# Kernel tuning notes

Measured on AMD Instinct MI355X. Metric: run time of the kernel, lower is better.

## Reference

```python
import jax, jax.numpy as jnp
import numpy as np

B, NPG, K, H = 64, 2048, 10, 64   # graphs, points-per-graph, kNN, hidden
N = B * NPG
EPS = 1e-5  # PairNorm eps


def _lin_init(key, fan_in, fan_out):
    kw, kb = jax.random.split(key)
    s = 1.0 / np.sqrt(fan_in)
    W = jax.random.uniform(kw, (fan_in, fan_out), jnp.float32, -s, s)
    b = jax.random.uniform(kb, (fan_out,), jnp.float32, -s, s)
    return W, b


def setup_inputs() -> dict:
    key = jax.random.key(0)
    ks = jax.random.split(key, 6)
    pos = jax.random.normal(ks[0], (N, 2), jnp.float32)
    batch = jnp.repeat(jnp.arange(B, dtype=jnp.int32), NPG)
    W1, b1 = _lin_init(ks[1], 2, H)
    W2, b2 = _lin_init(ks[2], H + 2, H)
    W3, b3 = _lin_init(ks[3], H + 2, H)
    Wl1, bl1 = _lin_init(ks[4], H, H)
    Wl2, bl2 = _lin_init(ks[5], H, 2)
    return dict(pos=pos, batch=batch, W1=W1, b1=b1, W2=W2, b2=b2,
                W3=W3, b3=b3, Wl1=Wl1, bl1=bl1, Wl2=Wl2, bl2=bl2)


def pair_norm(x):
    # PyG PairNorm, mode='PN', scale=1: center, then divide by rms of row norms
    xc = x - x.mean(axis=0, keepdims=True)
    return xc / jnp.sqrt(EPS + (xc ** 2).sum(axis=-1).mean())


def knn_edges(pos):
    # equal-sized graphs laid out contiguously -> batched pairwise distances
    p = pos.reshape(B, NPG, 2)
    d2 = ((p[:, :, None, :] - p[:, None, :, :]) ** 2).sum(-1)   # [B, n, n]
    d2 = jnp.where(jnp.eye(NPG, dtype=bool), jnp.inf, d2)       # loop=False
    _, idx = jax.lax.top_k(-d2, K)                              # [B, n, K]
    offs = (jnp.arange(NPG * B, step=NPG) if False else (jnp.arange(B) * NPG))[:, None, None]
    src = (idx + offs).reshape(-1)                              # neighbor j
    dst = jnp.broadcast_to(jnp.arange(N).reshape(B, NPG, 1), (B, NPG, K)).reshape(-1)
    # PointNetConv(add_self_loops=True): append self edges once, reuse in all convs
    sl = jnp.arange(N)
    return jnp.concatenate([src, sl]), jnp.concatenate([dst, sl])


def pointnet_conv(x, pos, src, dst, W, b):
    rel = pos[src] - pos[dst]                                    # [E, 2]
    msg = rel if x is None else jnp.concatenate([x[src], rel], axis=-1)
    msg = msg @ W + b                                            # local_nn
    return jax.ops.segment_max(msg, dst, num_segments=N)         # aggr='max'


def reference(pos, batch, W1, b1, W2, b2, W3, b3, Wl1, bl1, Wl2, bl2):
    src, dst = knn_edges(pos)
    h1 = pair_norm(jax.nn.relu(pointnet_conv(None, pos, src, dst, W1, b1)))
    h2 = pair_norm(jax.nn.relu(pointnet_conv(h1, pos, src, dst, W2, b2)))
    h3 = pair_norm(jax.nn.relu(pointnet_conv(h2, pos, src, dst, W3, b3)))
    g = h3.reshape(B, NPG, H).max(axis=1)                        # global_max_pool
    g = jax.nn.relu(g @ Wl1 + bl1)
    # dropout p=0.2 is identity in eval mode
    return g @ Wl2 + bl2                                         # [B, 2]
```

## Files before the change

### kernel.cpp

```cpp
#include <hip/hip_runtime.h>
#include <math.h>

#define NTOT   131072
#define NPG    2048
#define NB     64
#define KNNK   10
#define HID    64
#define EPSPN  1e-5f

__device__ inline float rdlane(float v, int l) {
    return __int_as_float(__builtin_amdgcn_readlane(__float_as_int(v), l));
}

__global__ __launch_bounds__(1024) void sort_kernel(const float2* __restrict__ pos,
        float2* __restrict__ spos, unsigned short* __restrict__ y2xg)
{
    __shared__ float2   sp[NPG];
    __shared__ unsigned sk[NPG];
    __shared__ unsigned sv[NPG];
    const int base = blockIdx.x * NPG;
    const int tid  = threadIdx.x;

    for (int t = tid; t < NPG; t += 1024) {
        unsigned u = __float_as_uint(pos[base + t].x);
        sk[t] = (u & 0x80000000u) ? ~u : (u | 0x80000000u);
        sv[t] = (unsigned)t;
    }
    __syncthreads();
    for (int k = 2; k <= NPG; k <<= 1) {
        for (int j = k >> 1; j > 0; j >>= 1) {
            int i = ((tid & ~(j - 1)) << 1) | (tid & (j - 1));
            int l = i + j;
            bool up = ((i & k) == 0);
            unsigned a = sk[i], b = sk[l];
            if ((a > b) == up) {
                sk[i] = b; sk[l] = a;
                unsigned t2 = sv[i]; sv[i] = sv[l]; sv[l] = t2;
            }
            __syncthreads();
        }
    }
    for (int t = tid; t < NPG; t += 1024) sp[t] = pos[base + sv[t]];
    __syncthreads();
    for (int t = tid; t < NPG; t += 1024) spos[base + t] = sp[t];

    for (int t = tid; t < NPG; t += 1024) {
        unsigned u = __float_as_uint(sp[t].y);
        sk[t] = (u & 0x80000000u) ? ~u : (u | 0x80000000u);
        sv[t] = (unsigned)t;
    }
    __syncthreads();
    for (int k = 2; k <= NPG; k <<= 1) {
        for (int j = k >> 1; j > 0; j >>= 1) {
            int i = ((tid & ~(j - 1)) << 1) | (tid & (j - 1));
            int l = i + j;
            bool up = ((i & k) == 0);
            unsigned a = sk[i], b = sk[l];
            if ((a > b) == up) {
                sk[i] = b; sk[l] = a;
                unsigned t2 = sv[i]; sv[i] = sv[l]; sv[l] = t2;
            }
            __syncthreads();
        }
    }
    for (int t = tid; t < NPG; t += 1024) y2xg[base + t] = (unsigned short)sv[t];
}

#define INSERT(INS, D2, JJ) do {                                              \
    const bool ins_ = (INS);                                                  \
    bd[9] = ins_ ? (D2) : bd[9];                                              \
    bi[9] = ins_ ? (JJ) : bi[9];                                              \
    _Pragma("unroll")                                                         \
    for (int kk = 0; kk < 9; ++kk) {                                          \
        bool sw_ = bd[kk] > bd[9];                                            \
        float tv_ = bd[kk]; int ti_ = bi[kk];                                 \
        bd[kk] = sw_ ? bd[9] : bd[kk]; bi[kk] = sw_ ? bi[9] : bi[kk];         \
        bd[9]  = sw_ ? tv_  : bd[9];   bi[9]  = sw_ ? ti_  : bi[9];           \
    }                                                                         \
} while (0)

#define CSWAP(A, B) do {                                                      \
    bool sw_ = bd[A] > bd[B];                                                 \
    float tf_ = bd[A]; int ti_ = bi[A];                                       \
    bd[A] = sw_ ? bd[B] : bd[A]; bi[A] = sw_ ? bi[B] : bi[A];                 \
    bd[B] = sw_ ? tf_  : bd[B]; bi[B] = sw_ ? ti_  : bi[B];                   \
} while (0)

__global__ __launch_bounds__(256) void knn_kernel(const float2* __restrict__ spos,
        const unsigned short* __restrict__ y2xg, unsigned short* __restrict__ knn)
{
    __shared__ float2 sarr[NPG];
    __shared__ unsigned short y2x[NPG];
    __shared__ unsigned short x2y[NPG];
    const int tid  = threadIdx.x;
    const int g    = blockIdx.x >> 4;
    const int base = g * NPG;

    for (int t = tid; t < NPG; t += 256) {
        sarr[t] = spos[base + t];
        y2x[t]  = y2xg[base + t];
    }
    __syncthreads();
    for (int t = tid; t < NPG; t += 256) {
        x2y[(int)y2x[t]] = (unsigned short)t;
    }
    __syncthreads();

    const int ql = ((blockIdx.x & 15) << 7) + (tid >> 1);
    const int d  = tid & 1;
    const float qx = sarr[ql].x, qy = sarr[ql].y;
    const int py = (int)x2y[ql];

    float span_x = sarr[min(ql + 8, NPG - 1)].x - sarr[max(ql - 8, 0)].x;
    float span_y = sarr[(int)y2x[min(py + 8, NPG - 1)]].y
                 - sarr[(int)y2x[max(py - 8, 0)]].y;
    const bool cy   = span_y > span_x;
    const int  r    = cy ? py : ql;
    const int  limit = d ? (NPG - 1 - r) : r;
    const int  sign  = d ? 1 : -1;

    float bd[KNNK];
    int   bi[KNNK];
#pragma unroll
    for (int k = 0; k < KNNK; ++k) { bd[k] = INFINITY; bi[k] = 0; }

    int s = 1;
    bool alive = (limit >= 1);
    while (__any(alive)) {
        int j0 = min(NPG - 1, max(0, r + sign * s));
        int j1 = min(NPG - 1, max(0, r + sign * (s + 1)));
        int j2 = min(NPG - 1, max(0, r + sign * (s + 2)));
        int j3 = min(NPG - 1, max(0, r + sign * (s + 3)));
        int x0 = cy ? (int)y2x[j0] : j0;
        int x1 = cy ? (int)y2x[j1] : j1;
        int x2 = cy ? (int)y2x[j2] : j2;
        int x3 = cy ? (int)y2x[j3] : j3;
        float2 p0 = sarr[x0];
        float2 p1 = sarr[x1];
        float2 p2 = sarr[x2];
        float2 p3 = sarr[x3];
        float dx0 = __fsub_rn(qx, p0.x), dy0 = __fsub_rn(qy, p0.y);
        float dx1 = __fsub_rn(qx, p1.x), dy1 = __fsub_rn(qy, p1.y);
        float dx2 = __fsub_rn(qx, p2.x), dy2 = __fsub_rn(qy, p2.y);
        float dx3 = __fsub_rn(qx, p3.x), dy3 = __fsub_rn(qy, p3.y);
        float xs0 = __fmul_rn(dx0, dx0), ys0 = __fmul_rn(dy0, dy0);
        float xs1 = __fmul_rn(dx1, dx1), ys1 = __fmul_rn(dy1, dy1);
        float xs2 = __fmul_rn(dx2, dx2), ys2 = __fmul_rn(dy2, dy2);
        float xs3 = __fmul_rn(dx3, dx3), ys3 = __fmul_rn(dy3, dy3);
        float d20 = __fadd_rn(xs0, ys0);
        float d21 = __fadd_rn(xs1, ys1);
        float d22 = __fadd_rn(xs2, ys2);
        float d23 = __fadd_rn(xs3, ys3);
        bool v0 = alive && (s     <= limit);
        bool v1 = alive && (s + 1 <= limit);
        bool v2 = alive && (s + 2 <= limit);
        bool v3 = alive && (s + 3 <= limit);
        bool pre = (v0 && d20 < bd[9]) || (v1 && d21 < bd[9]) ||
                   (v2 && d22 < bd[9]) || (v3 && d23 < bd[9]);
        if (__any(pre)) {
            INSERT(v0 && (d20 < bd[9]), d20, x0);
            INSERT(v1 && (d21 < bd[9]), d21, x1);
            INSERT(v2 && (d22 < bd[9]), d22, x2);
            INSERT(v3 && (d23 < bd[9]), d23, x3);
        }
        float thr = fminf(bd[9], __shfl_xor(bd[9], 1));
        float pr3 = cy ? ys3 : xs3;
        alive = alive && (s + 4 <= limit) && (pr3 < thr);
        s += 4;
    }

#pragma unroll
    for (int ph = 0; ph < 10; ++ph) {
        if ((ph & 1) == 0) { CSWAP(0,1); CSWAP(2,3); CSWAP(4,5); CSWAP(6,7); CSWAP(8,9); }
        else               { CSWAP(1,2); CSWAP(3,4); CSWAP(5,6); CSWAP(7,8); }
    }
    float obd[KNNK]; int obi[KNNK];
#pragma unroll
    for (int k = 0; k < KNNK; ++k) {
        obd[k] = __shfl_xor(bd[k], 1);
        obi[k] = __shfl_xor(bi[k], 1);
    }
    if (d == 0) {
        const int row = (base + ql) * KNNK;
#pragma unroll
        for (int k = 0; k < KNNK; ++k) {
            bool ta = bd[k] < obd[9 - k];
            int idx = ta ? bi[k] : obi[9 - k];
            knn[row + k] = (unsigned short)idx;
        }
    }
}

#define GEMM64(V, OUTEXPR) do {                                               \
    float a0 = 0.f, a1 = 0.f, a2 = 0.f, a3 = 0.f;                             \
    _Pragma("unroll")                                                         \
    for (int k = 0; k < 16; ++k) {                                            \
        a0 = fmaf(rdlane((V), k),      wcol[k],      a0);                     \
        a1 = fmaf(rdlane((V), k + 16), wcol[k + 16], a1);                     \
        a2 = fmaf(rdlane((V), k + 32), wcol[k + 32], a2);                     \
        a3 = fmaf(rdlane((V), k + 48), wcol[k + 48], a3);                     \
    }                                                                         \
    (OUTEXPR) = (a0 + a1) + (a2 + a3);                                        \
} while (0)

#define WSWZ() (((blockIdx.x & 7) << 7) | (blockIdx.x >> 3))

__global__ __launch_bounds__(256) void conv1_kernel(const float2* __restrict__ spos,
        const unsigned short* __restrict__ knn, const float* __restrict__ W1,
        const float* __restrict__ b1, const float* __restrict__ W2a,
        float* __restrict__ out, float* __restrict__ st)
{
    __shared__ float red[256];
    const int tid  = threadIdx.x;
    const int lane = tid & 63, w = tid >> 6;
    const int wg   = WSWZ();
    const int i0   = wg * 128 + w * 32;
    const int base = (wg >> 4) << 11;
    const float w0 = W1[lane], w1 = W1[HID + lane], bb = b1[lane];
    float wcol[HID];
#pragma unroll
    for (int k = 0; k < HID; ++k) wcol[k] = W2a[k * HID + lane];
    float cs = 0.f, ss = 0.f;
    for (int r = 0; r < 32; ++r) {
        const int i = i0 + r;
        float2 pi = spos[i];
        float acc = bb;
#pragma unroll
        for (int e = 0; e < KNNK; ++e) {
            int j = base + (int)knn[i * KNNK + e];
            float2 pj = spos[j];
            acc = fmaxf(acc, fmaf(pj.x - pi.x, w0, fmaf(pj.y - pi.y, w1, bb)));
        }
        float v = fmaxf(acc, 0.f);
        cs += v; ss = fmaf(v, v, ss);
        GEMM64(v, out[(size_t)i * HID + lane]);
    }
    red[tid] = cs; __syncthreads();
    if (tid < 64) atomicAdd(&st[tid], red[tid] + red[tid + 64] + red[tid + 128] + red[tid + 192]);
#pragma unroll
    for (int o = 32; o > 0; o >>= 1) ss += __shfl_xor(ss, o, 64);
    __syncthreads();
    if (lane == 0) red[w] = ss;
    __syncthreads();
    if (tid == 0) atomicAdd(&st[64], red[0] + red[1] + red[2] + red[3]);
}

__global__ __launch_bounds__(64) void stats_kernel(float* __restrict__ st,
        const float* __restrict__ Wn, const float* __restrict__ bn)
{
    const int c = threadIdx.x;
    float mean = st[c] * (1.0f / (float)NTOT);
    st[128 + c] = mean;
    float m2 = mean * mean;
#pragma unroll
    for (int o = 32; o > 0; o >>= 1) m2 += __shfl_xor(m2, o, 64);
    float s = (st[64] - (float)NTOT * m2) * (1.0f / (float)NTOT);
    s = fmaxf(s, 0.f);
    float inv = 1.0f / sqrtf(EPSPN + s);
    if (c == 0) st[66] = inv;
    if (Wn != nullptr) {
        float dot = 0.f;
#pragma unroll
        for (int k = 0; k < HID; ++k) dot = fmaf(rdlane(mean, k), Wn[k * HID + c], dot);
        st[192 + c] = bn[c] - inv * dot;
    }
}

__global__ __launch_bounds__(256, 2) void convG2_kernel(const float2* __restrict__ spos,
        const unsigned short* __restrict__ knn, const float* __restrict__ hw,
        const float* __restrict__ Wb, const float* __restrict__ Wna,
        const float* __restrict__ stin, float* __restrict__ out,
        float* __restrict__ stout)
{
    __shared__ float red[256];
    const int tid  = threadIdx.x;
    const int lane = tid & 63, w = tid >> 6;
    const int wg   = WSWZ();
    const int i0   = wg * 128 + w * 32;
    const int base = (wg >> 4) << 11;
    const float wb0 = Wb[lane], wb1 = Wb[HID + lane];
    const float inv = stin[66], offs = stin[192 + lane];
    float wcol[HID];
#pragma unroll
    for (int k = 0; k < HID; ++k) wcol[k] = Wna[k * HID + lane];

    const unsigned* kb = (const unsigned*)knn;
    unsigned idx0[5], idx1[5];
    float hwC[KNNK], hwN[KNNK];
#pragma unroll
    for (int e = 0; e < 5; ++e) idx0[e] = kb[(size_t)i0 * 5 + e];
#pragma unroll
    for (int e = 0; e < 5; ++e) idx1[e] = kb[(size_t)(i0 + 1) * 5 + e];
#pragma unroll
    for (int e = 0; e < 5; ++e) {
        int ja = base + (int)(idx0[e] & 0xFFFFu);
        int jb = base + (int)(idx0[e] >> 16);
        hwC[2 * e]     = hw[(size_t)ja * HID + lane];
        hwC[2 * e + 1] = hw[(size_t)jb * HID + lane];
    }

    float cs = 0.f, ss = 0.f;
    for (int r = 0; r < 32; ++r) {
        const int i = i0 + r;
        unsigned idx2[5];
        if (r + 2 < 32) {
#pragma unroll
            for (int e = 0; e < 5; ++e) idx2[e] = kb[(size_t)(i + 2) * 5 + e];
        }
        float2 pi = spos[i];
        float acc = fmaf(inv, hw[(size_t)i * HID + lane], offs);
#pragma unroll
        for (int e = 0; e < 5; ++e) {
            int ja = base + (int)(idx0[e] & 0xFFFFu);
            int jb = base + (int)(idx0[e] >> 16);
            float2 pa = spos[ja];
            float2 pb = spos[jb];
            float xwa = fmaf(inv, hwC[2 * e],     offs);
            float xwb = fmaf(inv, hwC[2 * e + 1], offs);
            acc = fmaxf(acc, fmaf(pa.x - pi.x, wb0, fmaf(pa.y - pi.y, wb1, xwa)));
            acc = fmaxf(acc, fmaf(pb.x - pi.x, wb0, fmaf(pb.y - pi.y, wb1, xwb)));
        }
        if (r + 1 < 32) {
#pragma unroll
            for (int e = 0; e < 5; ++e) {
                int ja = base + (int)(idx1[e] & 0xFFFFu);
                int jb = base + (int)(idx1[e] >> 16);
                hwN[2 * e]     = hw[(size_t)ja * HID + lane];
                hwN[2 * e + 1] = hw[(size_t)jb * HID + lane];
            }
        }
        float v = fmaxf(acc, 0.f);
        cs += v; ss = fmaf(v, v, ss);
        GEMM64(v, out[(size_t)i * HID + lane]);
#pragma unroll
        for (int e = 0; e < 5; ++e) idx0[e] = idx1[e];
        if (r + 2 < 32) {
#pragma unroll
            for (int e = 0; e < 5; ++e) idx1[e] = idx2[e];
        }
#pragma unroll
        for (int e = 0; e < KNNK; ++e) hwC[e] = hwN[e];
    }
    red[tid] = cs; __syncthreads();
    if (tid < 64) atomicAdd(&stout[tid], red[tid] + red[tid + 64] + red[tid + 128] + red[tid + 192]);
#pragma unroll
    for (int o = 32; o > 0; o >>= 1) ss += __shfl_xor(ss, o, 64);
    __syncthreads();
    if (lane == 0) red[w] = ss;
    __syncthreads();
    if (tid == 0) atomicAdd(&stout[64], red[0] + red[1] + red[2] + red[3]);
}

__global__ __launch_bounds__(256, 2) void convB3_kernel(const float2* __restrict__ spos,
        const unsigned short* __restrict__ knn, const float* __restrict__ hw,
        const float* __restrict__ Wb, const float* __restrict__ stin,
        float* __restrict__ stout, float* __restrict__ gmax)
{
    __shared__ float red[256];
    const int tid  = threadIdx.x;
    const int lane = tid & 63, w = tid >> 6;
    const int wg   = WSWZ();
    const int i0   = wg * 128 + w * 32;
    const int base = (wg >> 4) << 11;
    const float wb0 = Wb[lane], wb1 = Wb[HID + lane];
    const float inv = stin[66], offs = stin[192 + lane];

    const unsigned* kb = (const unsigned*)knn;
    unsigned idx0[5], idx1[5];
    float hwC[KNNK], hwN[KNNK];
#pragma unroll
    for (int e = 0; e < 5; ++e) idx0[e] = kb[(size_t)i0 * 5 + e];
#pragma unroll
    for (int e = 0; e < 5; ++e) idx1[e] = kb[(size_t)(i0 + 1) * 5 + e];
#pragma unroll
    for (int e = 0; e < 5; ++e) {
        int ja = base + (int)(idx0[e] & 0xFFFFu);
        int jb = base + (int)(idx0[e] >> 16);
        hwC[2 * e]     = hw[(size_t)ja * HID + lane];
        hwC[2 * e + 1] = hw[(size_t)jb * HID + lane];
    }

    float cs = 0.f, ss = 0.f, gm = 0.f;
    for (int r = 0; r < 32; ++r) {
        const int i = i0 + r;
        unsigned idx2[5];
        if (r + 2 < 32) {
#pragma unroll
            for (int e = 0; e < 5; ++e) idx2[e] = kb[(size_t)(i + 2) * 5 + e];
        }
        float2 pi = spos[i];
        float acc = fmaf(inv, hw[(size_t)i * HID + lane], offs);
#pragma unroll
        for (int e = 0; e < 5; ++e) {
            int ja = base + (int)(idx0[e] & 0xFFFFu);
            int jb = base + (int)(idx0[e] >> 16);
            float2 pa = spos[ja];
            float2 pb = spos[jb];
            float xwa = fmaf(inv, hwC[2 * e],     offs);
            float xwb = fmaf(inv, hwC[2 * e + 1], offs);
            acc = fmaxf(acc, fmaf(pa.x - pi.x, wb0, fmaf(pa.y - pi.y, wb1, xwa)));
            acc = fmaxf(acc, fmaf(pb.x - pi.x, wb0, fmaf(pb.y - pi.y, wb1, xwb)));
        }
        if (r + 1 < 32) {
#pragma unroll
            for (int e = 0; e < 5; ++e) {
                int ja = base + (int)(idx1[e] & 0xFFFFu);
                int jb = base + (int)(idx1[e] >> 16);
                hwN[2 * e]     = hw[(size_t)ja * HID + lane];
                hwN[2 * e + 1] = hw[(size_t)jb * HID + lane];
            }
        }
        float v = fmaxf(acc, 0.f);
        cs += v; ss = fmaf(v, v, ss);
        gm = fmaxf(gm, v);
#pragma unroll
        for (int e = 0; e < 5; ++e) idx0[e] = idx1[e];
        if (r + 2 < 32) {
#pragma unroll
            for (int e = 0; e < 5; ++e) idx1[e] = idx2[e];
        }
#pragma unroll
        for (int e = 0; e < KNNK; ++e) hwC[e] = hwN[e];
    }
    red[tid] = cs; __syncthreads();
    if (tid < 64) atomicAdd(&stout[tid], red[tid] + red[tid + 64] + red[tid + 128] + red[tid + 192]);
#pragma unroll
    for (int o = 32; o > 0; o >>= 1) ss += __shfl_xor(ss, o, 64);
    __syncthreads();
    if (lane == 0) red[w] = ss;
    __syncthreads();
    if (tid == 0) atomicAdd(&stout[64], red[0] + red[1] + red[2] + red[3]);
    const int g = (wg >> 4);
    atomicMax((int*)gmax + g * HID + lane, __float_as_int(gm));
}

__global__ __launch_bounds__(64) void head_kernel(const float* __restrict__ gmax,
        const float* __restrict__ st3, const float* __restrict__ Wl1,
        const float* __restrict__ bl1, const float* __restrict__ Wl2,
        const float* __restrict__ bl2, float* __restrict__ out)
{
    const int b = blockIdx.x, c = threadIdx.x;
    float gv = (gmax[b * HID + c] - st3[128 + c]) * st3[66];
    float a = bl1[c];
#pragma unroll
    for (int k = 0; k < HID; ++k) a = fmaf(rdlane(gv, k), Wl1[k * HID + c], a);
    float h1 = fmaxf(a, 0.f);
    float o = bl2[c & 1];
#pragma unroll
    for (int k = 0; k < HID; ++k) o = fmaf(rdlane(h1, k), Wl2[k * 2 + (c & 1)], o);
    if (c < 2) out[b * 2 + c] = o;
}

extern "C" void kernel_launch(void* const* d_in, const int* in_sizes, int n_in,
                              void* d_out, int out_size, void* d_ws, size_t ws_size,
                              hipStream_t stream)
{
    const float2* pos = (const float2*)d_in[0];
    const float* W1  = (const float*)d_in[2];
    const float* b1  = (const float*)d_in[3];
    const float* W2  = (const float*)d_in[4];
    const float* b2  = (const float*)d_in[5];
    const float* W3  = (const float*)d_in[6];
    const float* b3  = (const float*)d_in[7];
    const float* Wl1 = (const float*)d_in[8];
    const float* bl1 = (const float*)d_in[9];
    const float* Wl2 = (const float*)d_in[10];
    const float* bl2 = (const float*)d_in[11];
    float* out = (float*)d_out;

    char* p = (char*)d_ws;
    unsigned short* knn  = (unsigned short*)p;  p += (size_t)NTOT * KNNK * 2;
    float2* spos = (float2*)p;                  p += (size_t)NTOT * 8;
    unsigned short* y2xg = (unsigned short*)p;  p += (size_t)NTOT * 2;
    float* bufA  = (float*)p;                   p += (size_t)NTOT * HID * 4;
    float* bufB  = (float*)p;                   p += (size_t)NTOT * HID * 4;
    float* st    = (float*)p;
    float* gmax  = st + 768;

    hipMemsetAsync(st, 0, (768 + NB * HID) * sizeof(float), stream);

    sort_kernel<<<NB, 1024, 0, stream>>>(pos, spos, y2xg);
    knn_kernel <<<NTOT / 128, 256, 0, stream>>>(spos, y2xg, knn);

    conv1_kernel<<<NTOT / 128, 256, 0, stream>>>(spos, knn, W1, b1, W2, bufA, st);
    stats_kernel<<<1, 64, 0, stream>>>(st, W2, b2);

    convG2_kernel<<<NTOT / 128, 256, 0, stream>>>(spos, knn, bufA, W2 + 64 * HID,
                                                  W3, st, bufB, st + 256);
    stats_kernel<<<1, 64, 0, stream>>>(st + 256, W3, b3);

    convB3_kernel<<<NTOT / 128, 256, 0, stream>>>(spos, knn, bufB, W3 + 64 * HID,
                                                  st + 256, st + 512, gmax);
    stats_kernel<<<1, 64, 0, stream>>>(st + 512, nullptr, nullptr);

    head_kernel<<<NB, 64, 0, stream>>>(gmax, st + 512, Wl1, bl1, Wl2, bl2, out);
}
```

Baseline: 348.7 us.

## Split kNN sweep across four lanes per query with interleaved stride phases

Each query now uses four lanes instead of two: two directions times two interleaved phases, each phase stepping by eight along the sorted axis. The per-lane top-10 lists are combined with two sort-and-bitonic-min-merge rounds over xor-1 and xor-2 shuffles, and the grid doubles to 64 queries per block. The single batched insert check is also split into per-candidate wave-uniform insert guards. This shortens each lane's serial scan and adds parallelism, at the cost of restaging the whole graph's shared memory in twice as many blocks and doing an extra sort/merge.

```diff
diff --git a/kernel.cpp b/kernel.cpp
--- a/kernel.cpp
+++ b/kernel.cpp
@@ -86,6 +86,34 @@
     bd[B] = sw_ ? tf_  : bd[B]; bi[B] = sw_ ? ti_  : bi[B];                   \
 } while (0)
 
+#define SORT10() do {                                                         \
+    _Pragma("unroll")                                                         \
+    for (int ph_ = 0; ph_ < 10; ++ph_) {                                      \
+        if ((ph_ & 1) == 0) { CSWAP(0,1); CSWAP(2,3); CSWAP(4,5);             \
+                              CSWAP(6,7); CSWAP(8,9); }                       \
+        else                { CSWAP(1,2); CSWAP(3,4); CSWAP(5,6);             \
+                              CSWAP(7,8); }                                   \
+    }                                                                         \
+} while (0)
+
+#define MINMERGE(XORW) do {                                                   \
+    float obd[KNNK]; int obi[KNNK];                                           \
+    _Pragma("unroll")                                                         \
+    for (int k = 0; k < KNNK; ++k) {                                          \
+        obd[k] = __shfl_xor(bd[k], (XORW));                                   \
+        obi[k] = __shfl_xor(bi[k], (XORW));                                   \
+    }                                                                         \
+    float nbd[KNNK]; int nbi[KNNK];                                           \
+    _Pragma("unroll")                                                         \
+    for (int k = 0; k < KNNK; ++k) {                                          \
+        bool ta = bd[k] < obd[9 - k];                                         \
+        nbd[k] = ta ? bd[k] : obd[9 - k];                                     \
+        nbi[k] = ta ? bi[k] : obi[9 - k];                                     \
+    }                                                                         \
+    _Pragma("unroll")                                                         \
+    for (int k = 0; k < KNNK; ++k) { bd[k] = nbd[k]; bi[k] = nbi[k]; }        \
+} while (0)
+
 __global__ __launch_bounds__(256) void knn_kernel(const float2* __restrict__ spos,
         const unsigned short* __restrict__ y2xg, unsigned short* __restrict__ knn)
 {
@@ -93,7 +121,7 @@
     __shared__ unsigned short y2x[NPG];
     __shared__ unsigned short x2y[NPG];
     const int tid  = threadIdx.x;
-    const int g    = blockIdx.x >> 4;
+    const int g    = blockIdx.x >> 5;
     const int base = g * NPG;
 
     for (int t = tid; t < NPG; t += 256) {
@@ -106,8 +134,10 @@
     }
     __syncthreads();
 
-    const int ql = ((blockIdx.x & 15) << 7) + (tid >> 1);
-    const int d  = tid & 1;
+    const int ql = ((blockIdx.x & 31) << 6) + (tid >> 2);
+    const int d  = tid & 3;
+    const int dir = d & 1;
+    const int ph  = d >> 1;
     const float qx = sarr[ql].x, qy = sarr[ql].y;
     const int py = (int)x2y[ql];
 
@@ -116,8 +146,8 @@
                  - sarr[(int)y2x[max(py - 8, 0)]].y;
     const bool cy   = span_y > span_x;
     const int  r    = cy ? py : ql;
-    const int  limit = d ? (NPG - 1 - r) : r;
-    const int  sign  = d ? 1 : -1;
+    const int  limit = dir ? (NPG - 1 - r) : r;
+    const int  sign  = dir ? 1 : -1;
 
     float bd[KNNK];
     int   bi[KNNK];
@@ -125,12 +155,13 @@
     for (int k = 0; k < KNNK; ++k) { bd[k] = INFINITY; bi[k] = 0; }
 
     int s = 1;
-    bool alive = (limit >= 1);
+    bool alive = (4 * ph + 1 <= limit);
     while (__any(alive)) {
-        int j0 = min(NPG - 1, max(0, r + sign * s));
-        int j1 = min(NPG - 1, max(0, r + sign * (s + 1)));
-        int j2 = min(NPG - 1, max(0, r + sign * (s + 2)));
-        int j3 = min(NPG - 1, max(0, r + sign * (s + 3)));
+        const int o0 = s + 4 * ph;
+        int j0 = min(NPG - 1, max(0, r + sign * o0));
+        int j1 = min(NPG - 1, max(0, r + sign * (o0 + 1)));
+        int j2 = min(NPG - 1, max(0, r + sign * (o0 + 2)));
+        int j3 = min(NPG - 1, max(0, r + sign * (o0 + 3)));
         int x0 = cy ? (int)y2x[j0] : j0;
         int x1 = cy ? (int)y2x[j1] : j1;
         int x2 = cy ? (int)y2x[j2] : j2;
@@ -151,43 +182,36 @@
         float d21 = __fadd_rn(xs1, ys1);
         float d22 = __fadd_rn(xs2, ys2);
         float d23 = __fadd_rn(xs3, ys3);
-        bool v0 = alive && (s     <= limit);
-        bool v1 = alive && (s + 1 <= limit);
-        bool v2 = alive && (s + 2 <= limit);
-        bool v3 = alive && (s + 3 <= limit);
-        bool pre = (v0 && d20 < bd[9]) || (v1 && d21 < bd[9]) ||
-                   (v2 && d22 < bd[9]) || (v3 && d23 < bd[9]);
-        if (__any(pre)) {
-            INSERT(v0 && (d20 < bd[9]), d20, x0);
-            INSERT(v1 && (d21 < bd[9]), d21, x1);
-            INSERT(v2 && (d22 < bd[9]), d22, x2);
-            INSERT(v3 && (d23 < bd[9]), d23, x3);
-        }
+        bool v0 = alive && (o0     <= limit);
+        bool v1 = alive && (o0 + 1 <= limit);
+        bool v2 = alive && (o0 + 2 <= limit);
+        bool v3 = alive && (o0 + 3 <= limit);
+        bool c0 = v0 && (d20 < bd[9]);
+        if (__any(c0)) INSERT(c0, d20, x0);
+        bool c1 = v1 && (d21 < bd[9]);
+        if (__any(c1)) INSERT(c1, d21, x1);
+        bool c2 = v2 && (d22 < bd[9]);
+        if (__any(c2)) INSERT(c2, d22, x2);
+        bool c3 = v3 && (d23 < bd[9]);
+        if (__any(c3)) INSERT(c3, d23, x3);
+
         float thr = fminf(bd[9], __shfl_xor(bd[9], 1));
+        thr = fminf(thr, __shfl_xor(thr, 2));
         float pr3 = cy ? ys3 : xs3;
-        alive = alive && (s + 4 <= limit) && (pr3 < thr);
-        s += 4;
-    }
-
-#pragma unroll
-    for (int ph = 0; ph < 10; ++ph) {
-        if ((ph & 1) == 0) { CSWAP(0,1); CSWAP(2,3); CSWAP(4,5); CSWAP(6,7); CSWAP(8,9); }
-        else               { CSWAP(1,2); CSWAP(3,4); CSWAP(5,6); CSWAP(7,8); }
-    }
-    float obd[KNNK]; int obi[KNNK];
-#pragma unroll
-    for (int k = 0; k < KNNK; ++k) {
-        obd[k] = __shfl_xor(bd[k], 1);
-        obi[k] = __shfl_xor(bi[k], 1);
-    }
+        alive = alive && (o0 + 8 <= limit) && (pr3 < thr);
+        s += 8;
+    }
+
+    SORT10();
+    MINMERGE(1);
+    SORT10();
+    MINMERGE(2);
+
     if (d == 0) {
         const int row = (base + ql) * KNNK;
 #pragma unroll
-        for (int k = 0; k < KNNK; ++k) {
-            bool ta = bd[k] < obd[9 - k];
-            int idx = ta ? bi[k] : obi[9 - k];
-            knn[row + k] = (unsigned short)idx;
-        }
+        for (int k = 0; k < KNNK; ++k)
+            knn[row + k] = (unsigned short)bi[k];
     }
 }
 
@@ -480,7 +504,7 @@
     hipMemsetAsync(st, 0, (768 + NB * HID) * sizeof(float), stream);
 
     sort_kernel<<<NB, 1024, 0, stream>>>(pos, spos, y2xg);
-    knn_kernel <<<NTOT / 128, 256, 0, stream>>>(spos, y2xg, knn);
+    knn_kernel <<<NTOT / 64, 256, 0, stream>>>(spos, y2xg, knn);
 
     conv1_kernel<<<NTOT / 128, 256, 0, stream>>>(spos, knn, W1, b1, W2, bufA, st);
     stats_kernel<<<1, 64, 0, stream>>>(st, W2, b2);
```

Result: slower. 362.3 us (+3.9%).
